# Optimization experiments

Measured on AMD Instinct MI355X. Metric: run time of the kernel, lower is better.

## Reference

```python
import jax, jax.numpy as jnp
import numpy as np

B, NQ, NK = 4, 1024, 1024
DIM_Q, DIM_K, OUT_DIM, H = 512, 512, 512, 8
HEAD_DIM = OUT_DIM // H
SCALE = HEAD_DIM ** -0.5


def setup_inputs() -> dict:
    key = jax.random.key(0)
    ks = jax.random.split(key, 6)
    s_q = 1.0 / np.sqrt(DIM_Q)
    s_k = 1.0 / np.sqrt(DIM_K)
    s_o = 1.0 / np.sqrt(OUT_DIM)
    return {
        "x": jax.random.normal(ks[0], (B, NK, DIM_K), jnp.float32),
        "x_q": jax.random.normal(ks[1], (B, NQ, DIM_Q), jnp.float32),
        "w_q": jax.random.uniform(ks[2], (DIM_Q, OUT_DIM), jnp.float32, -s_q, s_q),
        "w_kv": jax.random.uniform(ks[3], (DIM_K, 2 * OUT_DIM), jnp.float32, -s_k, s_k),
        "w_proj": jax.random.uniform(ks[4], (OUT_DIM, OUT_DIM), jnp.float32, -s_o, s_o),
        "b_proj": jax.random.uniform(ks[5], (OUT_DIM,), jnp.float32, -s_o, s_o),
    }


def reference(x, x_q, w_q, w_kv, w_proj, b_proj):
    b, nk, _ = x.shape
    nq = x_q.shape[1]
    # q: [B,H,Nq,hd]
    q = (x_q @ w_q).reshape(b, nq, H, HEAD_DIM).transpose(0, 2, 1, 3)
    kv = (x @ w_kv).reshape(b, nk, 2, H, HEAD_DIM).transpose(2, 0, 3, 1, 4)
    k, v = kv[0], kv[1]  # each [B,H,Nk,hd]
    attn = jax.nn.softmax(jnp.einsum("bhqd,bhkd->bhqk", q, k) * SCALE, axis=-1)
    # dropout p=0.0 -> identity in both train and eval
    out = jnp.einsum("bhqk,bhkd->bqhd", attn, v).reshape(b, nq, OUT_DIM)
    out = out @ w_proj + b_proj
    return out, attn
```

## Files before the change

kernel.cpp:

```cpp
#include <hip/hip_runtime.h>

#define B_   4
#define NQ_  1024
#define NK_  1024
#define H_   8
#define DM_  512

typedef unsigned short us;
typedef unsigned long long ull;
typedef __attribute__((ext_vector_type(8))) short  short8;
typedef __attribute__((ext_vector_type(4))) float  f32x4;
typedef __attribute__((ext_vector_type(4))) int    i32x4;
typedef __attribute__((address_space(3))) unsigned int       lds_u32;
typedef const __attribute__((address_space(1))) unsigned int gl_u32;

static __device__ __forceinline__ us f2bf(float f) {
    unsigned int u = __builtin_bit_cast(unsigned int, f);
    u += 0x7FFF + ((u >> 16) & 1);
    return (us)(u >> 16);
}

__global__ __launch_bounds__(256) void wprep(
    const float* __restrict__ wq, const float* __restrict__ wkv,
    const float* __restrict__ wp,
    us* __restrict__ Wq_t, us* __restrict__ Wkv_t, us* __restrict__ Wp_t)
{
    const int t = blockIdx.x, tid = threadIdx.x;
    const float* src; us* dst; int k0, n0, N; const int K = 512;
    if (t < 64)       { src = wq;  dst = Wq_t;  N = 512;  k0 = (t >> 3) * 64;         n0 = (t & 7) * 64; }
    else if (t < 192) { src = wkv; dst = Wkv_t; N = 1024; k0 = ((t - 64) >> 4) * 64;  n0 = ((t - 64) & 15) * 64; }
    else              { src = wp;  dst = Wp_t;  N = 512;  k0 = ((t - 192) >> 3) * 64; n0 = ((t - 192) & 7) * 64; }

    __shared__ us T[64][72];
    #pragma unroll
    for (int i = 0; i < 4; ++i) {
        int s = tid + i * 256;
        int r = s >> 4, c4 = (s & 15) * 4;
        float4 v = *(const float4*)&src[(size_t)(k0 + r) * N + n0 + c4];
        T[r][c4 + 0] = f2bf(v.x); T[r][c4 + 1] = f2bf(v.y);
        T[r][c4 + 2] = f2bf(v.z); T[r][c4 + 3] = f2bf(v.w);
    }
    __syncthreads();
    #pragma unroll
    for (int i = 0; i < 2; ++i) {
        int s = tid + i * 256;
        int n = s >> 3, k8 = (s & 7) * 8;
        union { us u[8]; i32x4 v; } tmp;
        #pragma unroll
        for (int j = 0; j < 8; ++j) tmp.u[j] = T[k8 + j][n];
        *(i32x4*)&dst[(size_t)(n0 + n) * K + k0 + k8] = tmp.v;
    }
}

__device__ __forceinline__ void core128(const us* As, const us* Bs, int l, int w,
                                        f32x4 acc[4][4])
{
    const int wr = (w >> 1) * 64, wc = (w & 1) * 64;
    short8 af[4][2], bf_[4][2];
    #pragma unroll
    for (int rt = 0; rt < 4; ++rt) {
        int row = wr + rt * 16 + (l & 15);
        #pragma unroll
        for (int ks = 0; ks < 2; ++ks) {
            int slot = ks * 4 + (l >> 4);
            af[rt][ks] = *(const short8*)((const char*)As + row * 128 + ((slot ^ (row & 7)) * 16));
        }
    }
    #pragma unroll
    for (int ct = 0; ct < 4; ++ct) {
        int row = wc + ct * 16 + (l & 15);
        #pragma unroll
        for (int ks = 0; ks < 2; ++ks) {
            int slot = ks * 4 + (l >> 4);
            bf_[ct][ks] = *(const short8*)((const char*)Bs + row * 128 + ((slot ^ (row & 7)) * 16));
        }
    }
    #pragma unroll
    for (int ks = 0; ks < 2; ++ks)
        #pragma unroll
        for (int rt = 0; rt < 4; ++rt)
            #pragma unroll
            for (int ct = 0; ct < 4; ++ct)
                acc[rt][ct] = __builtin_amdgcn_mfma_f32_16x16x32_bf16(
                    af[rt][ks], bf_[ct][ks], acc[rt][ct], 0, 0, 0);
}

__global__ __launch_bounds__(256, 2) void qkv128(
    const float* __restrict__ x_q, const float* __restrict__ x,
    const us* __restrict__ Wq_t, const us* __restrict__ Wkv_t,
    us* __restrict__ Qh, us* __restrict__ Kpack, us* __restrict__ Vpack)
{
    const int z = blockIdx.z;
    const float* Af = z ? x : x_q;
    const us* Bt    = z ? Wkv_t : Wq_t;
    const int m0 = blockIdx.y * 128, n0 = blockIdx.x * 128;
    const int bn0 = n0 + (z == 2 ? 512 : 0);

    __shared__ us smem[16896];
    us* As = smem; us* Bs = smem + 8192;
    const int tid = threadIdx.x, l = tid & 63, w = tid >> 6;

    const int rr0 = w * 32 + (l >> 3);
    const int ss  = (l & 7) ^ ((l >> 3) & 7);
    const us* gB = Bt + (size_t)(bn0 + rr0) * 512 + ss * 8;
    const float* gA = Af + (size_t)(m0 + w * 32 + (l >> 4)) * 512 + (l & 15) * 4;

    f32x4 acc[4][4] = {};
    for (int k0 = 0; k0 < 512; k0 += 64) {
        #pragma unroll
        for (int i = 0; i < 4; ++i)
            __builtin_amdgcn_global_load_lds((gl_u32*)(gB + (size_t)i * 8 * 512 + k0),
                                             (lds_u32*)(Bs + (w * 32 + i * 8) * 64), 16, 0, 0);
        #pragma unroll
        for (int j = 0; j < 8; ++j) {
            float4 f = *(const float4*)(gA + (size_t)j * 4 * 512 + k0);
            int row = w * 32 + j * 4 + (l >> 4);
            ull pk = (ull)f2bf(f.x) | ((ull)f2bf(f.y) << 16)
                   | ((ull)f2bf(f.z) << 32) | ((ull)f2bf(f.w) << 48);
            int slot = (l & 15) >> 1, sub = l & 1;
            *(ull*)((char*)As + row * 128 + ((slot ^ (row & 7)) * 16) + sub * 8) = pk;
        }
        __syncthreads();
        core128(As, Bs, l, w, acc);
        __syncthreads();
    }

    const int wr = (w >> 1) * 64, wc = (w & 1) * 64;
    if (z == 0) {
        #pragma unroll
        for (int rt = 0; rt < 4; ++rt)
          #pragma unroll
          for (int ct = 0; ct < 4; ++ct)
            #pragma unroll
            for (int r = 0; r < 4; ++r) {
                int row = m0 + wr + rt * 16 + (l >> 4) * 4 + r;
                int col = n0 + wc + ct * 16 + (l & 15);
                int hh = col >> 6, d = col & 63;
                Qh[((size_t)((row >> 10) * H_ + hh) << 16) + (size_t)(row & 1023) * 64 + d]
                    = f2bf(acc[rt][ct][r] * 0.125f);
            }
    } else if (z == 1) {
        #pragma unroll
        for (int rt = 0; rt < 4; ++rt)
          #pragma unroll
          for (int ct = 0; ct < 4; ++ct)
            #pragma unroll
            for (int r = 0; r < 4; ++r) {
                int row = m0 + wr + rt * 16 + (l >> 4) * 4 + r;
                int col = n0 + wc + ct * 16 + (l & 15);
                int hh = col >> 6, d = col & 63;
                int bh = (row >> 10) * H_ + hh, tl = row & 1023;
                size_t byte = ((size_t)bh << 17) + (size_t)(tl >> 4) * 2048
                            + (size_t)(d >> 5) * 1024
                            + ((((d >> 3) & 3) * 16 + (tl & 15)) * 16) + (d & 7) * 2;
                *(us*)((char*)Kpack + byte) = f2bf(acc[rt][ct][r]);
            }
    } else {
        us* T = smem;
        #pragma unroll
        for (int rt = 0; rt < 4; ++rt)
          #pragma unroll
          for (int ct = 0; ct < 4; ++ct)
            #pragma unroll
            for (int r = 0; r < 4; ++r) {
                int rl = wr + rt * 16 + (l >> 4) * 4 + r;
                int cl = wc + ct * 16 + (l & 15);
                T[rl * 132 + cl] = f2bf(acc[rt][ct][r]);
            }
        __syncthreads();
        const int bb = m0 >> 10, tb = m0 & 1023;
        #pragma unroll
        for (int i = 0; i < 8; ++i) {
            int s = tid + i * 256;
            int col = s >> 4, r8 = (s & 15) * 8;
            union { us u[8]; i32x4 v; } tmp;
            #pragma unroll
            for (int j = 0; j < 8; ++j) tmp.u[j] = T[(r8 + j) * 132 + col];
            int gcol = n0 + col;
            int hh = gcol >> 6, d = gcol & 63;
            int bh = bb * H_ + hh;
            int tl0 = tb + r8;
            int dt = d >> 4, q = d & 15;
            int kt = tl0 >> 6, koff = tl0 & 63;
            int p = koff >> 5, q4 = (koff >> 3) & 3;
            size_t byte = ((size_t)bh << 17) + (size_t)((dt * 16 + kt) * 2 + p) * 1024
                        + (q4 * 16 + q) * 16;
            *(i32x4*)((char*)Vpack + byte) = tmp.v;
        }
    }
}

__global__ __launch_bounds__(256, 2) void out128(
    const us* __restrict__ Ob, const us* __restrict__ Wp_t,
    const float* __restrict__ bias, float* __restrict__ C)
{
    __shared__ us As[128 * 64], Bs[128 * 64];
    const int tid = threadIdx.x, l = tid & 63, w = tid >> 6;
    const int m0 = blockIdx.y * 128, n0 = blockIdx.x * 128;

    const int rr0 = w * 32 + (l >> 3);
    const int ss  = (l & 7) ^ ((l >> 3) & 7);
    const us* gA = Ob   + (size_t)(m0 + rr0) * 512 + ss * 8;
    const us* gB = Wp_t + (size_t)(n0 + rr0) * 512 + ss * 8;

    f32x4 acc[4][4] = {};
    for (int k0 = 0; k0 < 512; k0 += 64) {
        #pragma unroll
        for (int i = 0; i < 4; ++i) {
            __builtin_amdgcn_global_load_lds((gl_u32*)(gA + (size_t)i * 8 * 512 + k0),
                                             (lds_u32*)(As + (w * 32 + i * 8) * 64), 16, 0, 0);
            __builtin_amdgcn_global_load_lds((gl_u32*)(gB + (size_t)i * 8 * 512 + k0),
                                             (lds_u32*)(Bs + (w * 32 + i * 8) * 64), 16, 0, 0);
        }
        __syncthreads();
        core128(As, Bs, l, w, acc);
        __syncthreads();
    }

    const int wr = (w >> 1) * 64, wc = (w & 1) * 64;
    #pragma unroll
    for (int rt = 0; rt < 4; ++rt)
      #pragma unroll
      for (int ct = 0; ct < 4; ++ct)
        #pragma unroll
        for (int r = 0; r < 4; ++r) {
            int row = m0 + wr + rt * 16 + (l >> 4) * 4 + r;
            int col = n0 + wc + ct * 16 + (l & 15);
            __builtin_nontemporal_store(acc[rt][ct][r] + bias[col], &C[(size_t)row * 512 + col]);
        }
}

__global__ __launch_bounds__(512, 4) void attn5(
    const us* __restrict__ Qhp, const us* __restrict__ Kpack, const us* __restrict__ Vpack,
    float* __restrict__ attnOut, us* __restrict__ Ob)
{
    const int tid = threadIdx.x, lane = tid & 63, w = tid >> 6;
    const int rg = w >> 2, wk = w & 3;
    const int p = blockIdx.x + 32 * blockIdx.y + 256 * blockIdx.z;
    const int g = (p & 7) + 8 * ((p >> 3) & 3);
    const int b = g >> 3, h = g & 7, q0 = (p >> 5) * 32;
    const int q = lane & 15, q4 = lane >> 4;
    const int bh = b * H_ + h;

    __shared__ us P[32 * 1024];
    __shared__ float redM[2][4][16], redS[2][4][16];

    const us* qp = &Qhp[((size_t)bh << 16) + (size_t)(q0 + rg * 16 + q) * 64 + q4 * 8];
    short8 bq0 = *(const short8*)qp;
    short8 bq1 = *(const short8*)(qp + 32);

    const char* kb_base = (const char*)Kpack + ((size_t)bh << 17) + (size_t)wk * 16 * 2048 + lane * 16;

    f32x4 sv[16];
    #pragma unroll
    for (int ct = 0; ct < 16; ++ct) {
        const char* ka_ = kb_base + ct * 2048;
        short8 ka  = *(const short8*)ka_;
        short8 kb2 = *(const short8*)(ka_ + 1024);
        f32x4 a = {};
        a = __builtin_amdgcn_mfma_f32_16x16x32_bf16(ka, bq0, a, 0, 0, 0);
        a = __builtin_amdgcn_mfma_f32_16x16x32_bf16(kb2, bq1, a, 0, 0, 0);
        sv[ct] = a;
    }

    float m = sv[0][0];
    #pragma unroll
    for (int ct = 0; ct < 16; ++ct)
        #pragma unroll
        for (int r = 0; r < 4; ++r) m = fmaxf(m, sv[ct][r]);
    m = fmaxf(m, __shfl_xor(m, 16));
    m = fmaxf(m, __shfl_xor(m, 32));
    if (lane < 16) redM[rg][wk][lane] = m;
    __syncthreads();
    const float mg = fmaxf(fmaxf(redM[rg][0][q], redM[rg][1][q]),
                           fmaxf(redM[rg][2][q], redM[rg][3][q]));

    float s = 0.f;
    #pragma unroll
    for (int ct = 0; ct < 16; ++ct)
        #pragma unroll
        for (int r = 0; r < 4; ++r) {
            float e = __expf(sv[ct][r] - mg);
            sv[ct][r] = e;
            s += e;
        }
    s += __shfl_xor(s, 16);
    s += __shfl_xor(s, 32);
    if (lane < 16) redS[rg][wk][lane] = s;
    __syncthreads();
    const float inv = 1.0f / (redS[rg][0][q] + redS[rg][1][q] + redS[rg][2][q] + redS[rg][3][q]);

    const unsigned sw = (unsigned)(q & 7) << 4;
    #pragma unroll
    for (int ct = 0; ct < 16; ++ct) {
        const int key0 = wk * 256 + ct * 16 + q4 * 4;
        ull pk = (ull)f2bf(sv[ct][0] * inv)
               | ((ull)f2bf(sv[ct][1] * inv) << 16)
               | ((ull)f2bf(sv[ct][2] * inv) << 32)
               | ((ull)f2bf(sv[ct][3] * inv) << 48);
        unsigned byte = (unsigned)(rg * 16 + q) * 2048u + (((unsigned)(key0 * 2)) ^ sw);
        *(ull*)((char*)P + byte) = pk;
    }
    __syncthreads();

    const char* vbase = (const char*)Vpack + ((size_t)bh << 17)
                      + (size_t)wk * 32 * 1024 + lane * 16;
    short8 v0a = *(const short8*)(vbase);
    short8 v1a = *(const short8*)(vbase + 1024);

    {
        const size_t aRow = ((size_t)bh * NQ_ + q0) * NK_;
        #pragma unroll
        for (int i = 0; i < 4; ++i) {
            const int r = w * 4 + i;
            const unsigned swr = (unsigned)(r & 7) << 4;
            #pragma unroll
            for (int j = 0; j < 4; ++j) {
                unsigned byte = (unsigned)r * 2048u
                              + (((unsigned)(j * 512 + lane * 8)) ^ swr);
                ull pk = *(const ull*)((const char*)P + byte);
                f32x4 o;
                o[0] = __builtin_bit_cast(float, (unsigned)((pk & 0xFFFFull) << 16));
                o[1] = __builtin_bit_cast(float, (unsigned)(((pk >> 16) & 0xFFFFull) << 16));
                o[2] = __builtin_bit_cast(float, (unsigned)(((pk >> 32) & 0xFFFFull) << 16));
                o[3] = __builtin_bit_cast(float, (unsigned)((pk >> 48) << 16));
                __builtin_nontemporal_store(o,
                    (f32x4*)&attnOut[aRow + (size_t)r * NK_ + j * 256 + lane * 4]);
            }
        }
    }

    f32x4 acc0 = {}, acc1 = {};
    const unsigned prow = (unsigned)(rg * 16 + q) * 2048u;
    #pragma unroll
    for (int kt = 0; kt < 16; ++kt) {
        short8 vb0 = v0a, vb1 = v1a;
        if (kt < 15) {
            v0a = *(const short8*)(vbase + (kt + 1) * 2048);
            v1a = *(const short8*)(vbase + (kt + 1) * 2048 + 1024);
        }
        const int kb = kt * 64;
        unsigned o0 = ((unsigned)((kb + q4 * 8) * 2)) ^ sw;
        unsigned o1 = ((unsigned)((kb + 32 + q4 * 8) * 2)) ^ sw;
        short8 pa0 = *(const short8*)((const char*)P + prow + o0);
        short8 pa1 = *(const short8*)((const char*)P + prow + o1);
        __builtin_amdgcn_s_setprio(1);
        acc0 = __builtin_amdgcn_mfma_f32_16x16x32_bf16(pa0, vb0, acc0, 0, 0, 0);
        acc1 = __builtin_amdgcn_mfma_f32_16x16x32_bf16(pa1, vb1, acc1, 0, 0, 0);
        __builtin_amdgcn_s_setprio(0);
    }
    #pragma unroll
    for (int r = 0; r < 4; ++r) {
        float o = acc0[r] + acc1[r];
        Ob[(size_t)(b * NQ_ + q0 + rg * 16 + q4 * 4 + r) * 512 + h * 64 + wk * 16 + q] = f2bf(o);
    }
}

extern "C" void kernel_launch(void* const* d_in, const int* in_sizes, int n_in,
                              void* d_out, int out_size, void* d_ws, size_t ws_size,
                              hipStream_t stream)
{
    (void)in_sizes; (void)n_in; (void)out_size; (void)ws_size;
    const float* x    = (const float*)d_in[0];
    const float* x_q  = (const float*)d_in[1];
    const float* w_q  = (const float*)d_in[2];
    const float* w_kv = (const float*)d_in[3];
    const float* w_p  = (const float*)d_in[4];
    const float* b_p  = (const float*)d_in[5];

    float* out   = (float*)d_out;
    float* attnO = out + (size_t)B_ * NQ_ * DM_;

    us* Wq_t  = (us*)d_ws;
    us* Wkv_t = Wq_t  + 262144;
    us* Wp_t  = Wkv_t + 524288;
    us* Qh    = Wp_t  + 262144;
    us* Kp    = Qh    + 2097152;
    us* Vp    = Kp    + 2097152;
    us* Ob    = Vp    + 2097152;

    wprep<<<256, 256, 0, stream>>>(w_q, w_kv, w_p, Wq_t, Wkv_t, Wp_t);
    qkv128<<<dim3(4, 32, 3), 256, 0, stream>>>(x_q, x, Wq_t, Wkv_t, Qh, Kp, Vp);
    attn5<<<dim3(32, 8, 4), 512, 0, stream>>>(Qh, Kp, Vp, attnO, Ob);
    out128<<<dim3(4, 32), 256, 0, stream>>>(Ob, Wp_t, b_p, out);
}
```

Before: 83.44 us.

## Double-buffer projection GEMMs with 128x64 tiles and tweak attention priorities

The QKV and output projection GEMMs move from 128x128 tiles with single-buffered LDS to 128x64 tiles with two LDS buffers. The next k-slice is prefetched while MFMAs run on the current one, and one barrier per iteration is dropped. The smaller N tile doubles the grid, from 384 to 768 blocks for QKV and from 128 to 256 for the output projection, to improve CU occupancy, at the cost of reloading the A tile more often. The attention kernel also raises wave priority around the QK MFMAs and uses nontemporal stores for its bf16 output.

Result: slower. 86.47 us (+3.6%).

```diff
diff --git a/kernel.cpp b/kernel.cpp
--- a/kernel.cpp
+++ b/kernel.cpp
@@ -52,11 +52,11 @@
     }
 }
 
-__device__ __forceinline__ void core128(const us* As, const us* Bs, int l, int w,
-                                        f32x4 acc[4][4])
-{
-    const int wr = (w >> 1) * 64, wc = (w & 1) * 64;
-    short8 af[4][2], bf_[4][2];
+__device__ __forceinline__ void core6432(const us* As, const us* Bs, int l, int w,
+                                         f32x4 acc[4][2])
+{
+    const int wr = (w >> 1) * 64, wc = (w & 1) * 32;
+    short8 af[4][2], bf_[2][2];
     #pragma unroll
     for (int rt = 0; rt < 4; ++rt) {
         int row = wr + rt * 16 + (l & 15);
@@ -67,7 +67,7 @@
         }
     }
     #pragma unroll
-    for (int ct = 0; ct < 4; ++ct) {
+    for (int ct = 0; ct < 2; ++ct) {
         int row = wc + ct * 16 + (l & 15);
         #pragma unroll
         for (int ks = 0; ks < 2; ++ks) {
@@ -80,7 +80,7 @@
         #pragma unroll
         for (int rt = 0; rt < 4; ++rt)
             #pragma unroll
-            for (int ct = 0; ct < 4; ++ct)
+            for (int ct = 0; ct < 2; ++ct)
                 acc[rt][ct] = __builtin_amdgcn_mfma_f32_16x16x32_bf16(
                     af[rt][ks], bf_[ct][ks], acc[rt][ct], 0, 0, 0);
 }
@@ -93,49 +93,75 @@
     const int z = blockIdx.z;
     const float* Af = z ? x : x_q;
     const us* Bt    = z ? Wkv_t : Wq_t;
-    const int m0 = blockIdx.y * 128, n0 = blockIdx.x * 128;
+    const int m0 = blockIdx.y * 128, n0 = blockIdx.x * 64;
     const int bn0 = n0 + (z == 2 ? 512 : 0);
-
-    __shared__ us smem[16896];
-    us* As = smem; us* Bs = smem + 8192;
+    const int hh = blockIdx.x;
+
+    __shared__ us smem[24576];
+    us* As0 = smem;          us* Bs0 = smem + 8192;
+    us* As1 = smem + 12288;  us* Bs1 = smem + 20480;
     const int tid = threadIdx.x, l = tid & 63, w = tid >> 6;
 
-    const int rr0 = w * 32 + (l >> 3);
-    const int ss  = (l & 7) ^ ((l >> 3) & 7);
-    const us* gB = Bt + (size_t)(bn0 + rr0) * 512 + ss * 8;
+    const us* gB = Bt + (size_t)(bn0 + w * 8 + (l >> 3)) * 512 + (size_t)(((l & 7) ^ (l >> 3)) * 8);
     const float* gA = Af + (size_t)(m0 + w * 32 + (l >> 4)) * 512 + (l & 15) * 4;
 
-    f32x4 acc[4][4] = {};
-    for (int k0 = 0; k0 < 512; k0 += 64) {
-        #pragma unroll
-        for (int i = 0; i < 4; ++i)
-            __builtin_amdgcn_global_load_lds((gl_u32*)(gB + (size_t)i * 8 * 512 + k0),
-                                             (lds_u32*)(Bs + (w * 32 + i * 8) * 64), 16, 0, 0);
-        #pragma unroll
-        for (int j = 0; j < 8; ++j) {
-            float4 f = *(const float4*)(gA + (size_t)j * 4 * 512 + k0);
-            int row = w * 32 + j * 4 + (l >> 4);
-            ull pk = (ull)f2bf(f.x) | ((ull)f2bf(f.y) << 16)
-                   | ((ull)f2bf(f.z) << 32) | ((ull)f2bf(f.w) << 48);
-            int slot = (l & 15) >> 1, sub = l & 1;
-            *(ull*)((char*)As + row * 128 + ((slot ^ (row & 7)) * 16) + sub * 8) = pk;
+    float4 ar[8];
+    f32x4 acc[4][2] = {};
+
+    #pragma unroll
+    for (int i = 0; i < 2; ++i)
+        __builtin_amdgcn_global_load_lds((gl_u32*)(gB + (size_t)i * 32 * 512),
+                                         (lds_u32*)(Bs0 + (w * 8 + i * 32) * 64), 16, 0, 0);
+    #pragma unroll
+    for (int j = 0; j < 8; ++j) ar[j] = *(const float4*)(gA + (size_t)j * 4 * 512);
+    #pragma unroll
+    for (int j = 0; j < 8; ++j) {
+        int row = w * 32 + j * 4 + (l >> 4);
+        ull pk = (ull)f2bf(ar[j].x) | ((ull)f2bf(ar[j].y) << 16)
+               | ((ull)f2bf(ar[j].z) << 32) | ((ull)f2bf(ar[j].w) << 48);
+        int slot = (l & 15) >> 1, sub = l & 1;
+        *(ull*)((char*)As0 + row * 128 + ((slot ^ (row & 7)) * 16) + sub * 8) = pk;
+    }
+    __syncthreads();
+
+    for (int t = 0; t < 8; ++t) {
+        us* Ascur = (t & 1) ? As1 : As0;
+        us* Bscur = (t & 1) ? Bs1 : Bs0;
+        us* Asnxt = (t & 1) ? As0 : As1;
+        us* Bsnxt = (t & 1) ? Bs0 : Bs1;
+        if (t < 7) {
+            const int k1 = (t + 1) * 64;
+            #pragma unroll
+            for (int i = 0; i < 2; ++i)
+                __builtin_amdgcn_global_load_lds((gl_u32*)(gB + (size_t)i * 32 * 512 + k1),
+                                                 (lds_u32*)(Bsnxt + (w * 8 + i * 32) * 64), 16, 0, 0);
+            #pragma unroll
+            for (int j = 0; j < 8; ++j) ar[j] = *(const float4*)(gA + (size_t)j * 4 * 512 + k1);
+        }
+        core6432(Ascur, Bscur, l, w, acc);
+        if (t < 7) {
+            #pragma unroll
+            for (int j = 0; j < 8; ++j) {
+                int row = w * 32 + j * 4 + (l >> 4);
+                ull pk = (ull)f2bf(ar[j].x) | ((ull)f2bf(ar[j].y) << 16)
+                       | ((ull)f2bf(ar[j].z) << 32) | ((ull)f2bf(ar[j].w) << 48);
+                int slot = (l & 15) >> 1, sub = l & 1;
+                *(ull*)((char*)Asnxt + row * 128 + ((slot ^ (row & 7)) * 16) + sub * 8) = pk;
+            }
         }
         __syncthreads();
-        core128(As, Bs, l, w, acc);
-        __syncthreads();
-    }
-
-    const int wr = (w >> 1) * 64, wc = (w & 1) * 64;
+    }
+
+    const int wr = (w >> 1) * 64, wc = (w & 1) * 32;
     if (z == 0) {
         #pragma unroll
         for (int rt = 0; rt < 4; ++rt)
           #pragma unroll
-          for (int ct = 0; ct < 4; ++ct)
+          for (int ct = 0; ct < 2; ++ct)
             #pragma unroll
             for (int r = 0; r < 4; ++r) {
                 int row = m0 + wr + rt * 16 + (l >> 4) * 4 + r;
-                int col = n0 + wc + ct * 16 + (l & 15);
-                int hh = col >> 6, d = col & 63;
+                int d   = wc + ct * 16 + (l & 15);
                 Qh[((size_t)((row >> 10) * H_ + hh) << 16) + (size_t)(row & 1023) * 64 + d]
                     = f2bf(acc[rt][ct][r] * 0.125f);
             }
@@ -143,12 +169,11 @@
         #pragma unroll
         for (int rt = 0; rt < 4; ++rt)
           #pragma unroll
-          for (int ct = 0; ct < 4; ++ct)
+          for (int ct = 0; ct < 2; ++ct)
             #pragma unroll
             for (int r = 0; r < 4; ++r) {
                 int row = m0 + wr + rt * 16 + (l >> 4) * 4 + r;
-                int col = n0 + wc + ct * 16 + (l & 15);
-                int hh = col >> 6, d = col & 63;
+                int d   = wc + ct * 16 + (l & 15);
                 int bh = (row >> 10) * H_ + hh, tl = row & 1023;
                 size_t byte = ((size_t)bh << 17) + (size_t)(tl >> 4) * 2048
                             + (size_t)(d >> 5) * 1024
@@ -160,29 +185,27 @@
         #pragma unroll
         for (int rt = 0; rt < 4; ++rt)
           #pragma unroll
-          for (int ct = 0; ct < 4; ++ct)
+          for (int ct = 0; ct < 2; ++ct)
             #pragma unroll
             for (int r = 0; r < 4; ++r) {
                 int rl = wr + rt * 16 + (l >> 4) * 4 + r;
                 int cl = wc + ct * 16 + (l & 15);
-                T[rl * 132 + cl] = f2bf(acc[rt][ct][r]);
+                T[rl * 68 + cl] = f2bf(acc[rt][ct][r]);
             }
         __syncthreads();
         const int bb = m0 >> 10, tb = m0 & 1023;
-        #pragma unroll
-        for (int i = 0; i < 8; ++i) {
+        const int bh = bb * H_ + hh;
+        #pragma unroll
+        for (int i = 0; i < 4; ++i) {
             int s = tid + i * 256;
-            int col = s >> 4, r8 = (s & 15) * 8;
+            int d = s & 63, kg = s >> 6;
             union { us u[8]; i32x4 v; } tmp;
             #pragma unroll
-            for (int j = 0; j < 8; ++j) tmp.u[j] = T[(r8 + j) * 132 + col];
-            int gcol = n0 + col;
-            int hh = gcol >> 6, d = gcol & 63;
-            int bh = bb * H_ + hh;
-            int tl0 = tb + r8;
+            for (int j = 0; j < 8; ++j) tmp.u[j] = T[(kg * 8 + j) * 68 + d];
+            int key0 = tb + kg * 8;
+            int kt = key0 >> 6, koff = key0 & 63;
+            int p = koff >> 5, q4 = (koff >> 3) & 3;
             int dt = d >> 4, q = d & 15;
-            int kt = tl0 >> 6, koff = tl0 & 63;
-            int p = koff >> 5, q4 = (koff >> 3) & 3;
             size_t byte = ((size_t)bh << 17) + (size_t)((dt * 16 + kt) * 2 + p) * 1024
                         + (q4 * 16 + q) * 16;
             *(i32x4*)((char*)Vpack + byte) = tmp.v;
@@ -194,34 +217,52 @@
     const us* __restrict__ Ob, const us* __restrict__ Wp_t,
     const float* __restrict__ bias, float* __restrict__ C)
 {
-    __shared__ us As[128 * 64], Bs[128 * 64];
+    __shared__ us smem[24576];
+    us* As0 = smem;          us* Bs0 = smem + 8192;
+    us* As1 = smem + 12288;  us* Bs1 = smem + 20480;
     const int tid = threadIdx.x, l = tid & 63, w = tid >> 6;
-    const int m0 = blockIdx.y * 128, n0 = blockIdx.x * 128;
-
-    const int rr0 = w * 32 + (l >> 3);
-    const int ss  = (l & 7) ^ ((l >> 3) & 7);
-    const us* gA = Ob   + (size_t)(m0 + rr0) * 512 + ss * 8;
-    const us* gB = Wp_t + (size_t)(n0 + rr0) * 512 + ss * 8;
-
-    f32x4 acc[4][4] = {};
-    for (int k0 = 0; k0 < 512; k0 += 64) {
-        #pragma unroll
-        for (int i = 0; i < 4; ++i) {
-            __builtin_amdgcn_global_load_lds((gl_u32*)(gA + (size_t)i * 8 * 512 + k0),
-                                             (lds_u32*)(As + (w * 32 + i * 8) * 64), 16, 0, 0);
-            __builtin_amdgcn_global_load_lds((gl_u32*)(gB + (size_t)i * 8 * 512 + k0),
-                                             (lds_u32*)(Bs + (w * 32 + i * 8) * 64), 16, 0, 0);
-        }
+    const int m0 = blockIdx.y * 128, n0 = blockIdx.x * 64;
+
+    const us* gA = Ob   + (size_t)(m0 + w * 32 + (l >> 3)) * 512 + (size_t)(((l & 7) ^ (l >> 3)) * 8);
+    const us* gB = Wp_t + (size_t)(n0 + w * 8  + (l >> 3)) * 512 + (size_t)(((l & 7) ^ (l >> 3)) * 8);
+
+    f32x4 acc[4][2] = {};
+
+    #pragma unroll
+    for (int i = 0; i < 4; ++i)
+        __builtin_amdgcn_global_load_lds((gl_u32*)(gA + (size_t)i * 8 * 512),
+                                         (lds_u32*)(As0 + (w * 32 + i * 8) * 64), 16, 0, 0);
+    #pragma unroll
+    for (int i = 0; i < 2; ++i)
+        __builtin_amdgcn_global_load_lds((gl_u32*)(gB + (size_t)i * 32 * 512),
+                                         (lds_u32*)(Bs0 + (w * 8 + i * 32) * 64), 16, 0, 0);
+    __syncthreads();
+
+    for (int t = 0; t < 8; ++t) {
+        us* Ascur = (t & 1) ? As1 : As0;
+        us* Bscur = (t & 1) ? Bs1 : Bs0;
+        us* Asnxt = (t & 1) ? As0 : As1;
+        us* Bsnxt = (t & 1) ? Bs0 : Bs1;
+        if (t < 7) {
+            const int k1 = (t + 1) * 64;
+            #pragma unroll
+            for (int i = 0; i < 4; ++i)
+                __builtin_amdgcn_global_load_lds((gl_u32*)(gA + (size_t)i * 8 * 512 + k1),
+                                                 (lds_u32*)(Asnxt + (w * 32 + i * 8) * 64), 16, 0, 0);
+            #pragma unroll
+            for (int i = 0; i < 2; ++i)
+                __builtin_amdgcn_global_load_lds((gl_u32*)(gB + (size_t)i * 32 * 512 + k1),
+                                                 (lds_u32*)(Bsnxt + (w * 8 + i * 32) * 64), 16, 0, 0);
+        }
+        core6432(Ascur, Bscur, l, w, acc);
         __syncthreads();
-        core128(As, Bs, l, w, acc);
-        __syncthreads();
-    }
-
-    const int wr = (w >> 1) * 64, wc = (w & 1) * 64;
+    }
+
+    const int wr = (w >> 1) * 64, wc = (w & 1) * 32;
     #pragma unroll
     for (int rt = 0; rt < 4; ++rt)
       #pragma unroll
-      for (int ct = 0; ct < 4; ++ct)
+      for (int ct = 0; ct < 2; ++ct)
         #pragma unroll
         for (int r = 0; r < 4; ++r) {
             int row = m0 + wr + rt * 16 + (l >> 4) * 4 + r;
@@ -230,7 +271,7 @@
         }
 }
 
-__global__ __launch_bounds__(512, 4) void attn5(
+__global__ __launch_bounds__(512, 4) void attn6(
     const us* __restrict__ Qhp, const us* __restrict__ Kpack, const us* __restrict__ Vpack,
     float* __restrict__ attnOut, us* __restrict__ Ob)
 {
@@ -258,8 +299,10 @@
         short8 ka  = *(const short8*)ka_;
         short8 kb2 = *(const short8*)(ka_ + 1024);
         f32x4 a = {};
+        __builtin_amdgcn_s_setprio(1);
         a = __builtin_amdgcn_mfma_f32_16x16x32_bf16(ka, bq0, a, 0, 0, 0);
         a = __builtin_amdgcn_mfma_f32_16x16x32_bf16(kb2, bq1, a, 0, 0, 0);
+        __builtin_amdgcn_s_setprio(0);
         sv[ct] = a;
     }
 
@@ -352,7 +395,8 @@
     #pragma unroll
     for (int r = 0; r < 4; ++r) {
         float o = acc0[r] + acc1[r];
-        Ob[(size_t)(b * NQ_ + q0 + rg * 16 + q4 * 4 + r) * 512 + h * 64 + wk * 16 + q] = f2bf(o);
+        __builtin_nontemporal_store(f2bf(o),
+            &Ob[(size_t)(b * NQ_ + q0 + rg * 16 + q4 * 4 + r) * 512 + h * 64 + wk * 16 + q]);
     }
 }
 
@@ -380,7 +424,7 @@
     us* Ob    = Vp    + 2097152;
 
     wprep<<<256, 256, 0, stream>>>(w_q, w_kv, w_p, Wq_t, Wkv_t, Wp_t);
-    qkv128<<<dim3(4, 32, 3), 256, 0, stream>>>(x_q, x, Wq_t, Wkv_t, Qh, Kp, Vp);
-    attn5<<<dim3(32, 8, 4), 512, 0, stream>>>(Qh, Kp, Vp, attnO, Ob);
-    out128<<<dim3(4, 32), 256, 0, stream>>>(Ob, Wp_t, b_p, out);
-}
+    qkv128<<<dim3(8, 32, 3), 256, 0, stream>>>(x_q, x, Wq_t, Wkv_t, Qh, Kp, Vp);
+    attn6<<<dim3(32, 8, 4), 512, 0, stream>>>(Qh, Kp, Vp, attnO, Ob);
+    out128<<<dim3(8, 32), 256, 0, stream>>>(Ob, Wp_t, b_p, out);
+}
```
